# Optimization experiments

Hardware: AMD Instinct MI355X
Metric: run time of the kernel (lower is better)

## Reference

```python
import jax, jax.numpy as jnp
import numpy as np

T, B, M, H = 2048, 16, 512, 256
R_MIN, R_MAX, MAX_PHASE = 0.0, 1.0, 6.28


def setup_inputs() -> dict:
    key = jax.random.key(0)
    ks = jax.random.split(key, 10)
    inputs = jax.random.normal(ks[0], (T, B, M), dtype=jnp.float32)
    h_re = jnp.zeros((B, H), dtype=jnp.float32)
    h_im = jnp.zeros((B, H), dtype=jnp.float32)
    # parameter inits matching the torch module (stable |lambda| < 1)
    u1 = jax.random.uniform(ks[1], (H,), dtype=jnp.float32)
    nu_log = jnp.log(-0.5 * jnp.log(u1 * (R_MAX**2 - R_MIN**2) + R_MIN**2))
    u2 = jax.random.uniform(ks[2], (H,), dtype=jnp.float32)
    theta_log = jnp.log(MAX_PHASE * u2)
    lam = jnp.exp(-jnp.exp(nu_log) + 1j * jnp.exp(theta_log))
    gamma_log = jnp.log(jnp.sqrt(1.0 - jnp.abs(lam) ** 2))
    B_re = jax.random.normal(ks[3], (H, M), dtype=jnp.float32) / np.sqrt(2 * M)
    B_im = jax.random.normal(ks[4], (H, M), dtype=jnp.float32) / np.sqrt(2 * M)
    C_re = jax.random.normal(ks[5], (M, H), dtype=jnp.float32) / np.sqrt(H)
    C_im = jax.random.normal(ks[6], (M, H), dtype=jnp.float32) / np.sqrt(H)
    D = jax.random.normal(ks[7], (M,), dtype=jnp.float32)
    return {"inputs": inputs, "h_re": h_re, "h_im": h_im,
            "nu_log": nu_log, "theta_log": theta_log, "gamma_log": gamma_log,
            "B_re": B_re, "B_im": B_im, "C_re": C_re, "C_im": C_im, "D": D}


def reference(inputs, h_re, h_im, nu_log, theta_log, gamma_log,
              B_re, B_im, C_re, C_im, D):
    # diag_lambda = exp(-exp(nu) + i exp(theta)), shape [H]
    lam = jnp.exp(jnp.complex64(-jnp.exp(nu_log) + 1j * jnp.exp(theta_log)))
    B_norm = (B_re + 1j * B_im) * jnp.exp(gamma_log)[:, None]  # [H, M] complex
    C = C_re + 1j * C_im                                        # [M, H] complex
    h0 = (h_re + 1j * h_im).astype(jnp.complex64)               # [B, H]
    Bu = inputs.astype(jnp.complex64) @ B_norm.T                # [T, B, H] precomputed input drive

    def step(h, xs):
        bu_t, x_t = xs
        h = h * lam + bu_t                                      # [B, H]
        y = jnp.real(h @ C.T) + D * x_t                         # [B, M]
        return h, y

    h_final, outputs = jax.lax.scan(step, h0, (Bu, inputs))
    return outputs, h_final
```

## Files before the change

### kernel.cpp

```cpp
#include <hip/hip_runtime.h>
#include <hip/hip_bf16.h>
#include <math.h>

#define T_DIM 2048
#define B_DIM 16
#define M_DIM 512
#define H_DIM 256
#define KC 512
#define K_DIM 512
#define CHUNK 64
#define NCHUNK 32
#define NTILE 16

typedef unsigned short ushort_t;
typedef __attribute__((ext_vector_type(8))) short short8;
typedef __attribute__((ext_vector_type(8))) unsigned short ushort8;
typedef __attribute__((ext_vector_type(4))) float f32x4;

#define WS_CARRY 0
#define WS_WB_BF 262144
#define WS_WC_BF 393216
#define WS_XB    524288
#define WS_BU    8912896

__device__ inline int tidx(int n, int k) {
    return (((n >> 7) * 16 + (k >> 5)) << 12) + (((k >> 3) & 3) << 10)
         + ((n & 127) << 3) + (k & 7);
}

__device__ inline ushort_t f2bf(float f) {
    __hip_bfloat16 h = __float2bfloat16(f);
    return *reinterpret_cast<ushort_t*>(&h);
}
__device__ inline float bf2f(ushort_t u) {
    union { unsigned int i; float f; } v;
    v.i = ((unsigned int)u) << 16;
    return v.f;
}

__global__ __launch_bounds__(256) void prep_all(
        const float* __restrict__ X, ushort_t* __restrict__ Xb,
        const float* __restrict__ B_re, const float* __restrict__ B_im,
        const float* __restrict__ gamma_log,
        const float* __restrict__ C_re, const float* __restrict__ C_im,
        ushort_t* __restrict__ wb, ushort_t* __restrict__ wc) {
    int bid = blockIdx.x;
    if (bid < 8192) {
        int f = bid * 256 + threadIdx.x;
        int n = f >> 6, ko = f & 63;
        const float* p = X + (size_t)n * 512 + ko * 8;
        float4 a = *(const float4*)p;
        float4 b = *(const float4*)(p + 4);
        ushort8 u;
        u[0] = f2bf(a.x); u[1] = f2bf(a.y); u[2] = f2bf(a.z); u[3] = f2bf(a.w);
        u[4] = f2bf(b.x); u[5] = f2bf(b.y); u[6] = f2bf(b.z); u[7] = f2bf(b.w);
        *(ushort8*)(&Xb[(((n >> 7) * 16 + (ko >> 2)) << 12) + ((ko & 3) << 10)
                        + ((n & 127) << 3)]) = u;
    } else {
        int idx = (bid - 8192) * 256 + threadIdx.x;
        int e    = idx & 7;
        int slot = (idx >> 3) & 511;
        int row  = slot & 127;
        int ks   = slot >> 7;
        int t    = (idx >> 12) & 15;
        int blk  = idx >> 16;
        int j = blk * 128 + row;
        int k = t * 32 + ks * 8 + e;
        float v;
        if (j < 256) v = expf(gamma_log[j])       * B_re[j * 512 + k];
        else         v = expf(gamma_log[j - 256]) * B_im[(j - 256) * 512 + k];
        wb[idx] = f2bf(v);
        float w;
        if (k < 256) w =  C_re[j * 256 + k];
        else         w = -C_im[j * 256 + (k - 256)];
        wc[idx] = f2bf(w);
    }
}

template <int MODE>
__global__ __launch_bounds__(512) void gemm_mfma(
    const ushort_t* __restrict__ A, const ushort_t* __restrict__ W,
    void* __restrict__ Cv, const float* __restrict__ Dv,
    const ushort_t* __restrict__ Xb) {
    __shared__ ushort_t Asl[2][4][4096];
    __shared__ ushort_t Bsl[2][4][4096];
    const int tid = threadIdx.x;
    const int id = blockIdx.x;
    const int rb = ((id >> 4) << 3) + (id & 7);
    const int nb = (id >> 3) & 1;
    const int bm = rb << 8, bn = nb << 8;
    const int lane = tid & 63, wid = tid >> 6;
    const int wr  = (wid >> 2) << 7;
    const int wcc = (wid & 3) << 6;
    const int l16 = lane & 15, ksl = lane >> 4;

    f32x4 acc[MODE == 0 ? 4 : 8][MODE == 0 ? 8 : 4] = {};

    auto stage = [&](int t, int buf) {
#pragma unroll
        for (int q = 0; q < 2; ++q) {
#pragma unroll
            for (int kk = 0; kk < 2; ++kk) {
                size_t ab = ((size_t)((2 * rb + q) * NTILE + (2 * t + kk))) * 4096;
                __builtin_amdgcn_global_load_lds(
                    (const __attribute__((address_space(1))) void*)(A + ab + tid * 8),
                    (__attribute__((address_space(3))) void*)(&Asl[buf][q * 2 + kk][tid * 8]),
                    16, 0, 0);
                size_t bb = ((size_t)((2 * nb + q) * NTILE + (2 * t + kk))) * 4096;
                __builtin_amdgcn_global_load_lds(
                    (const __attribute__((address_space(1))) void*)(W + bb + tid * 8),
                    (__attribute__((address_space(3))) void*)(&Bsl[buf][q * 2 + kk][tid * 8]),
                    16, 0, 0);
            }
        }
    };

    stage(0, 0);
    __syncthreads();

    int cur = 0;
#pragma unroll 2
    for (int t = 0; t < 8; ++t) {
        const int nxt = cur ^ 1;
        if (t + 1 < 8) stage(t + 1, nxt);
#pragma unroll
        for (int kk = 0; kk < 2; ++kk) {
            short8 afr[8], bfr[4];
#pragma unroll
            for (int m = 0; m < 8; ++m) {
                int row = wr + m * 16 + l16;
                afr[m] = *(const short8*)(&Asl[cur][(row >> 7) * 2 + kk]
                                              [ksl * 1024 + (row & 127) * 8]);
            }
#pragma unroll
            for (int n = 0; n < 4; ++n) {
                int col = wcc + n * 16 + l16;
                bfr[n] = *(const short8*)(&Bsl[cur][(col >> 7) * 2 + kk]
                                              [ksl * 1024 + (col & 127) * 8]);
            }
            if constexpr (MODE == 0) {
#pragma unroll
                for (int i = 0; i < 4; ++i)
#pragma unroll
                    for (int j = 0; j < 8; ++j)
                        acc[i][j] = __builtin_amdgcn_mfma_f32_16x16x32_bf16(
                            bfr[i], afr[j], acc[i][j], 0, 0, 0);
            } else {
#pragma unroll
                for (int i = 0; i < 8; ++i)
#pragma unroll
                    for (int j = 0; j < 4; ++j)
                        acc[i][j] = __builtin_amdgcn_mfma_f32_16x16x32_bf16(
                            afr[i], bfr[j], acc[i][j], 0, 0, 0);
            }
        }
        __syncthreads();
        cur = nxt;
    }

    const int fr = (lane >> 4) << 2;
    if constexpr (MODE == 0) {
        ushort_t* Bu = (ushort_t*)Cv;
#pragma unroll
        for (int i = 0; i < 4; ++i) {
            int k0 = bn + wcc + i * 16 + fr;
#pragma unroll
            for (int j = 0; j < 8; ++j) {
                int n = bm + wr + j * 16 + l16;
                uint2 p;
                p.x = (unsigned int)f2bf(acc[i][j][0])
                    | ((unsigned int)f2bf(acc[i][j][1]) << 16);
                p.y = (unsigned int)f2bf(acc[i][j][2])
                    | ((unsigned int)f2bf(acc[i][j][3]) << 16);
                size_t off = ((size_t)((n >> 7) * 16 + (k0 >> 5)) << 12)
                           + (((k0 >> 3) & 3) << 10) + ((n & 127) << 3) + (k0 & 7);
                *(uint2*)(&Bu[off]) = p;
            }
        }
    } else {
#pragma unroll
        for (int i = 0; i < 8; ++i) {
#pragma unroll
            for (int j = 0; j < 4; ++j) {
#pragma unroll
                for (int r = 0; r < 4; ++r) {
                    int row = bm + wr + i * 16 + fr + r;
                    int col = bn + wcc + j * 16 + l16;
                    size_t o = (size_t)row * 512 + col;
                    ((float*)Cv)[o] = acc[i][j][r] + Dv[col] * bf2f(Xb[tidx(row, col)]);
                }
            }
        }
    }
}

__global__ __launch_bounds__(256) void scan_local(const float* __restrict__ nu_log,
        const float* __restrict__ theta_log, float* __restrict__ ws) {
    const int c = blockIdx.x;
    const int s = blockIdx.y;
    const int b = threadIdx.x >> 4;
    const int h0 = s * 32 + (threadIdx.x & 15) * 2;
    float lr[2], li[2];
#pragma unroll
    for (int q = 0; q < 2; ++q) {
        float nu = expf(nu_log[h0 + q]);
        float th = expf(theta_log[h0 + q]);
        float r  = expf(-nu);
        lr[q] = r * cosf(th); li[q] = r * sinf(th);
    }
    const ushort_t* Bu = (const ushort_t*)(ws + WS_BU);
    float hr[2] = {0.f, 0.f}, hi[2] = {0.f, 0.f};
    for (int l0 = 0; l0 < CHUNK; l0 += 8) {
        unsigned int vre[8], vim[8];
#pragma unroll
        for (int u = 0; u < 8; ++u) {
            int n = (c * CHUNK + l0 + u) * B_DIM + b;
            vre[u] = *(const unsigned int*)(&Bu[tidx(n, h0)]);
            vim[u] = *(const unsigned int*)(&Bu[tidx(n, h0 + 256)]);
        }
#pragma unroll
        for (int u = 0; u < 8; ++u) {
#pragma unroll
            for (int q = 0; q < 2; ++q) {
                float br = bf2f((ushort_t)(q ? (vre[u] >> 16) : (vre[u] & 0xffff)));
                float bi = bf2f((ushort_t)(q ? (vim[u] >> 16) : (vim[u] & 0xffff)));
                float nr = fmaf(lr[q], hr[q], fmaf(-li[q], hi[q], br));
                float ni = fmaf(lr[q], hi[q], fmaf(li[q], hr[q], bi));
                hr[q] = nr; hi[q] = ni;
            }
        }
    }
    size_t cb = (size_t)(c * B_DIM + b) * KC;
    *(float2*)(&ws[WS_CARRY + cb + h0])       = make_float2(hr[0], hr[1]);
    *(float2*)(&ws[WS_CARRY + cb + 256 + h0]) = make_float2(hi[0], hi[1]);
}

__global__ __launch_bounds__(256) void scan_carry(const float* __restrict__ nu_log,
        const float* __restrict__ theta_log, float* __restrict__ ws,
        const float* __restrict__ h_re, const float* __restrict__ h_im,
        float* __restrict__ out, int out_size) {
    const int b = blockIdx.x;
    const int h = threadIdx.x;
    const float nu = expf(nu_log[h]);
    const float th = expf(theta_log[h]);
    const float rL  = expf(-64.f * nu);
    const float thL = 64.f * th;
    const float Lr = rL * cosf(thL), Li = rL * sinf(thL);
    float cr = h_re[b * H_DIM + h], ci = h_im[b * H_DIM + h];
    for (int c = 0; c < NCHUNK; ++c) {
        size_t cidx = ((size_t)(c * B_DIM + b)) * KC + h;
        float sr = ws[WS_CARRY + cidx], si = ws[WS_CARRY + cidx + 256];
        ws[WS_CARRY + cidx]       = cr;
        ws[WS_CARRY + cidx + 256] = ci;
        float nr = fmaf(Lr, cr, fmaf(-Li, ci, sr));
        float ni = fmaf(Lr, ci, fmaf(Li, cr, si));
        cr = nr; ci = ni;
    }
    const size_t base = (size_t)T_DIM * B_DIM * M_DIM;
    const size_t idx  = (size_t)b * H_DIM + h;
    size_t ore = base + idx;
    size_t oim = base + (size_t)B_DIM * H_DIM + idx;
    if (ore < (size_t)out_size) out[ore] = cr;
    if (oim < (size_t)out_size) out[oim] = ci;
}

__global__ __launch_bounds__(256) void scan_apply(const float* __restrict__ nu_log,
        const float* __restrict__ theta_log, float* __restrict__ ws) {
    const int c = blockIdx.x;
    const int s = blockIdx.y;
    const int b = threadIdx.x >> 4;
    const int h0 = s * 32 + (threadIdx.x & 15) * 2;
    float lr[2], li[2];
#pragma unroll
    for (int q = 0; q < 2; ++q) {
        float nu = expf(nu_log[h0 + q]);
        float th = expf(theta_log[h0 + q]);
        float r  = expf(-nu);
        lr[q] = r * cosf(th); li[q] = r * sinf(th);
    }
    ushort_t* Bu = (ushort_t*)(ws + WS_BU);
    size_t cb = (size_t)(c * B_DIM + b) * KC;
    float2 f2r = *(const float2*)(&ws[WS_CARRY + cb + h0]);
    float2 f2i = *(const float2*)(&ws[WS_CARRY + cb + 256 + h0]);
    float hr[2] = {f2r.x, f2r.y}, hi[2] = {f2i.x, f2i.y};
    for (int l0 = 0; l0 < CHUNK; l0 += 8) {
        unsigned int vre[8], vim[8];
        int ire[8], iim[8];
#pragma unroll
        for (int u = 0; u < 8; ++u) {
            int n = (c * CHUNK + l0 + u) * B_DIM + b;
            ire[u] = tidx(n, h0);
            iim[u] = tidx(n, h0 + 256);
            vre[u] = *(const unsigned int*)(&Bu[ire[u]]);
            vim[u] = *(const unsigned int*)(&Bu[iim[u]]);
        }
#pragma unroll
        for (int u = 0; u < 8; ++u) {
#pragma unroll
            for (int q = 0; q < 2; ++q) {
                float br = bf2f((ushort_t)(q ? (vre[u] >> 16) : (vre[u] & 0xffff)));
                float bi = bf2f((ushort_t)(q ? (vim[u] >> 16) : (vim[u] & 0xffff)));
                float nr = fmaf(lr[q], hr[q], fmaf(-li[q], hi[q], br));
                float ni = fmaf(lr[q], hi[q], fmaf(li[q], hr[q], bi));
                hr[q] = nr; hi[q] = ni;
            }
            *(unsigned int*)(&Bu[ire[u]]) =
                (unsigned int)f2bf(hr[0]) | ((unsigned int)f2bf(hr[1]) << 16);
            *(unsigned int*)(&Bu[iim[u]]) =
                (unsigned int)f2bf(hi[0]) | ((unsigned int)f2bf(hi[1]) << 16);
        }
    }
}

extern "C" void kernel_launch(void* const* d_in, const int* in_sizes, int n_in,
                              void* d_out, int out_size, void* d_ws, size_t ws_size,
                              hipStream_t stream) {
    const float* inputs    = (const float*)d_in[0];
    const float* h_re      = (const float*)d_in[1];
    const float* h_im      = (const float*)d_in[2];
    const float* nu_log    = (const float*)d_in[3];
    const float* theta_log = (const float*)d_in[4];
    const float* gamma_log = (const float*)d_in[5];
    const float* B_re      = (const float*)d_in[6];
    const float* B_im      = (const float*)d_in[7];
    const float* C_re      = (const float*)d_in[8];
    const float* C_im      = (const float*)d_in[9];
    const float* Dv        = (const float*)d_in[10];
    float* out = (float*)d_out;
    float* ws  = (float*)d_ws;
    ushort_t* wb = (ushort_t*)(ws + WS_WB_BF);
    ushort_t* wc = (ushort_t*)(ws + WS_WC_BF);
    ushort_t* xb = (ushort_t*)(ws + WS_XB);
    ushort_t* bu = (ushort_t*)(ws + WS_BU);

    prep_all<<<9216, 256, 0, stream>>>(inputs, xb, B_re, B_im, gamma_log,
                                       C_re, C_im, wb, wc);

    gemm_mfma<0><<<256, 512, 0, stream>>>(xb, wb, (void*)bu, nullptr, nullptr);

    scan_local<<<dim3(NCHUNK, 8), 256, 0, stream>>>(nu_log, theta_log, ws);
    scan_carry<<<B_DIM, 256, 0, stream>>>(nu_log, theta_log, ws, h_re, h_im,
                                          out, out_size);
    scan_apply<<<dim3(NCHUNK, 8), 256, 0, stream>>>(nu_log, theta_log, ws);

    gemm_mfma<1><<<256, 512, 0, stream>>>(bu, wc, (void*)out, Dv, xb);
}
```

Measured before the change: 102.1 us.

## Fuse fp32-to-bf16 input conversion into first GEMM's A-tile load

Removes the separate pass that converted the fp32 inputs into a tiled bf16 copy. The first GEMM now loads fp32 input rows into registers, converts them to bf16 and writes them to LDS itself, with the register loads overlapped with the MFMA work of the current tile. The second GEMM's D*x skip term now reads the original fp32 inputs instead of the bf16 copy. This saves a full write and re-read of the converted activations and one kernel's worth of traffic, at the cost of register-staged loads in place of direct global-to-LDS loads and extra VALU conversion inside the GEMM.

```diff
diff --git a/kernel.cpp b/kernel.cpp
--- a/kernel.cpp
+++ b/kernel.cpp
@@ -20,7 +20,6 @@
 #define WS_CARRY 0
 #define WS_WB_BF 262144
 #define WS_WC_BF 393216
-#define WS_XB    524288
 #define WS_BU    8912896
 
 __device__ inline int tidx(int n, int k) {
@@ -38,50 +37,34 @@
     return v.f;
 }
 
-__global__ __launch_bounds__(256) void prep_all(
-        const float* __restrict__ X, ushort_t* __restrict__ Xb,
-        const float* __restrict__ B_re, const float* __restrict__ B_im,
-        const float* __restrict__ gamma_log,
-        const float* __restrict__ C_re, const float* __restrict__ C_im,
-        ushort_t* __restrict__ wb, ushort_t* __restrict__ wc) {
-    int bid = blockIdx.x;
-    if (bid < 8192) {
-        int f = bid * 256 + threadIdx.x;
-        int n = f >> 6, ko = f & 63;
-        const float* p = X + (size_t)n * 512 + ko * 8;
-        float4 a = *(const float4*)p;
-        float4 b = *(const float4*)(p + 4);
-        ushort8 u;
-        u[0] = f2bf(a.x); u[1] = f2bf(a.y); u[2] = f2bf(a.z); u[3] = f2bf(a.w);
-        u[4] = f2bf(b.x); u[5] = f2bf(b.y); u[6] = f2bf(b.z); u[7] = f2bf(b.w);
-        *(ushort8*)(&Xb[(((n >> 7) * 16 + (ko >> 2)) << 12) + ((ko & 3) << 10)
-                        + ((n & 127) << 3)]) = u;
-    } else {
-        int idx = (bid - 8192) * 256 + threadIdx.x;
-        int e    = idx & 7;
-        int slot = (idx >> 3) & 511;
-        int row  = slot & 127;
-        int ks   = slot >> 7;
-        int t    = (idx >> 12) & 15;
-        int blk  = idx >> 16;
-        int j = blk * 128 + row;
-        int k = t * 32 + ks * 8 + e;
-        float v;
-        if (j < 256) v = expf(gamma_log[j])       * B_re[j * 512 + k];
-        else         v = expf(gamma_log[j - 256]) * B_im[(j - 256) * 512 + k];
-        wb[idx] = f2bf(v);
-        float w;
-        if (k < 256) w =  C_re[j * 256 + k];
-        else         w = -C_im[j * 256 + (k - 256)];
-        wc[idx] = f2bf(w);
-    }
+__global__ void prep_w(const float* __restrict__ B_re, const float* __restrict__ B_im,
+                       const float* __restrict__ gamma_log,
+                       const float* __restrict__ C_re, const float* __restrict__ C_im,
+                       ushort_t* __restrict__ wb, ushort_t* __restrict__ wc) {
+    int idx = blockIdx.x * blockDim.x + threadIdx.x;
+    int e    = idx & 7;
+    int slot = (idx >> 3) & 511;
+    int row  = slot & 127;
+    int ks   = slot >> 7;
+    int t    = (idx >> 12) & 15;
+    int blk  = idx >> 16;
+    int j = blk * 128 + row;
+    int k = t * 32 + ks * 8 + e;
+    float v;
+    if (j < 256) v = expf(gamma_log[j])       * B_re[j * 512 + k];
+    else         v = expf(gamma_log[j - 256]) * B_im[(j - 256) * 512 + k];
+    wb[idx] = f2bf(v);
+    float w;
+    if (k < 256) w =  C_re[j * 256 + k];
+    else         w = -C_im[j * 256 + (k - 256)];
+    wc[idx] = f2bf(w);
 }
 
 template <int MODE>
 __global__ __launch_bounds__(512) void gemm_mfma(
-    const ushort_t* __restrict__ A, const ushort_t* __restrict__ W,
+    const void* __restrict__ Aptr, const ushort_t* __restrict__ W,
     void* __restrict__ Cv, const float* __restrict__ Dv,
-    const ushort_t* __restrict__ Xb) {
+    const float* __restrict__ X) {
     __shared__ ushort_t Asl[2][4][4096];
     __shared__ ushort_t Bsl[2][4][4096];
     const int tid = threadIdx.x;
@@ -94,35 +77,76 @@
     const int wcc = (wid & 3) << 6;
     const int l16 = lane & 15, ksl = lane >> 4;
 
+    const ushort_t* At = (const ushort_t*)Aptr;
+    const float*    Xf = (const float*)Aptr;
+
+    const int ar  = tid >> 1;
+    const int akh = (tid & 1) << 5;
+    const int asub = ((ar >> 7) << 1) + (tid & 1);
+    const int arow127 = ar & 127;
+
     f32x4 acc[MODE == 0 ? 4 : 8][MODE == 0 ? 8 : 4] = {};
-
-    auto stage = [&](int t, int buf) {
-#pragma unroll
-        for (int q = 0; q < 2; ++q) {
+    float4 av[8];
+
+    auto stageB = [&](int t, int buf) {
+#pragma unroll
+        for (int q = 0; q < 2; ++q)
 #pragma unroll
             for (int kk = 0; kk < 2; ++kk) {
-                size_t ab = ((size_t)((2 * rb + q) * NTILE + (2 * t + kk))) * 4096;
-                __builtin_amdgcn_global_load_lds(
-                    (const __attribute__((address_space(1))) void*)(A + ab + tid * 8),
-                    (__attribute__((address_space(3))) void*)(&Asl[buf][q * 2 + kk][tid * 8]),
-                    16, 0, 0);
                 size_t bb = ((size_t)((2 * nb + q) * NTILE + (2 * t + kk))) * 4096;
                 __builtin_amdgcn_global_load_lds(
                     (const __attribute__((address_space(1))) void*)(W + bb + tid * 8),
                     (__attribute__((address_space(3))) void*)(&Bsl[buf][q * 2 + kk][tid * 8]),
                     16, 0, 0);
             }
-        }
     };
-
-    stage(0, 0);
+    auto stageA = [&](int t, int buf) {
+#pragma unroll
+        for (int q = 0; q < 2; ++q)
+#pragma unroll
+            for (int kk = 0; kk < 2; ++kk) {
+                size_t ab = ((size_t)((2 * rb + q) * NTILE + (2 * t + kk))) * 4096;
+                __builtin_amdgcn_global_load_lds(
+                    (const __attribute__((address_space(1))) void*)(At + ab + tid * 8),
+                    (__attribute__((address_space(3))) void*)(&Asl[buf][q * 2 + kk][tid * 8]),
+                    16, 0, 0);
+            }
+    };
+    auto loadA = [&](int t) {
+        const float* p = Xf + (size_t)(bm + ar) * 512 + t * 64 + akh;
+#pragma unroll
+        for (int i = 0; i < 8; ++i) av[i] = *(const float4*)(p + i * 4);
+    };
+    auto writeA = [&](int buf) {
+#pragma unroll
+        for (int i = 0; i < 4; ++i) {
+            float4 a = av[2 * i], b = av[2 * i + 1];
+            ushort8 u;
+            u[0] = f2bf(a.x); u[1] = f2bf(a.y); u[2] = f2bf(a.z); u[3] = f2bf(a.w);
+            u[4] = f2bf(b.x); u[5] = f2bf(b.y); u[6] = f2bf(b.z); u[7] = f2bf(b.w);
+            *(ushort8*)(&Asl[buf][asub][(i * 128 + arow127) * 8]) = u;
+        }
+    };
+
+    if constexpr (MODE == 0) {
+        stageB(0, 0);
+        loadA(0);
+        writeA(0);
+    } else {
+        stageA(0, 0);
+        stageB(0, 0);
+    }
     __syncthreads();
 
     int cur = 0;
 #pragma unroll 2
     for (int t = 0; t < 8; ++t) {
         const int nxt = cur ^ 1;
-        if (t + 1 < 8) stage(t + 1, nxt);
+        if (t + 1 < 8) {
+            stageB(t + 1, nxt);
+            if constexpr (MODE == 0) loadA(t + 1);
+            else                     stageA(t + 1, nxt);
+        }
 #pragma unroll
         for (int kk = 0; kk < 2; ++kk) {
             short8 afr[8], bfr[4];
@@ -154,6 +178,7 @@
                             afr[i], bfr[j], acc[i][j], 0, 0, 0);
             }
         }
+        if constexpr (MODE == 0) { if (t + 1 < 8) writeA(nxt); }
         __syncthreads();
         cur = nxt;
     }
@@ -187,7 +212,7 @@
                     int row = bm + wr + i * 16 + fr + r;
                     int col = bn + wcc + j * 16 + l16;
                     size_t o = (size_t)row * 512 + col;
-                    ((float*)Cv)[o] = acc[i][j][r] + Dv[col] * bf2f(Xb[tidx(row, col)]);
+                    ((float*)Cv)[o] = acc[i][j][r] + Dv[col] * X[o];
                 }
             }
         }
@@ -330,18 +355,16 @@
     float* ws  = (float*)d_ws;
     ushort_t* wb = (ushort_t*)(ws + WS_WB_BF);
     ushort_t* wc = (ushort_t*)(ws + WS_WC_BF);
-    ushort_t* xb = (ushort_t*)(ws + WS_XB);
     ushort_t* bu = (ushort_t*)(ws + WS_BU);
 
-    prep_all<<<9216, 256, 0, stream>>>(inputs, xb, B_re, B_im, gamma_log,
-                                       C_re, C_im, wb, wc);
-
-    gemm_mfma<0><<<256, 512, 0, stream>>>(xb, wb, (void*)bu, nullptr, nullptr);
+    prep_w<<<1024, 256, 0, stream>>>(B_re, B_im, gamma_log, C_re, C_im, wb, wc);
+
+    gemm_mfma<0><<<256, 512, 0, stream>>>(inputs, wb, (void*)bu, nullptr, inputs);
 
     scan_local<<<dim3(NCHUNK, 8), 256, 0, stream>>>(nu_log, theta_log, ws);
     scan_carry<<<B_DIM, 256, 0, stream>>>(nu_log, theta_log, ws, h_re, h_im,
                                           out, out_size);
     scan_apply<<<dim3(NCHUNK, 8), 256, 0, stream>>>(nu_log, theta_log, ws);
 
-    gemm_mfma<1><<<256, 512, 0, stream>>>(bu, wc, (void*)out, Dv, xb);
-}
+    gemm_mfma<1><<<256, 512, 0, stream>>>(bu, wc, (void*)out, Dv, inputs);
+}
```

New measurement: 103.7 us. Within noise of the previous version (+1.6%).

## Fuse chunk-carry propagation into scan_apply, removing the serial carry kernel

Applied to the files above, without the earlier changes.

Removes the separate scan_carry kernel that walked the 32 chunk summaries serially per batch. Each scan_apply block now recomputes its own incoming carry by folding all preceding chunk summaries with lambda^64, and the last chunk writes the final hidden state. This saves a kernel launch and a serial dependency stage. In exchange it adds redundant carry work, up to 31 steps for later chunks, and makes the load uneven across blocks.

```diff
diff --git a/kernel.cpp b/kernel.cpp
--- a/kernel.cpp
+++ b/kernel.cpp
@@ -235,54 +235,44 @@
     *(float2*)(&ws[WS_CARRY + cb + 256 + h0]) = make_float2(hi[0], hi[1]);
 }
 
-__global__ __launch_bounds__(256) void scan_carry(const float* __restrict__ nu_log,
+__global__ __launch_bounds__(256) void scan_apply(const float* __restrict__ nu_log,
         const float* __restrict__ theta_log, float* __restrict__ ws,
         const float* __restrict__ h_re, const float* __restrict__ h_im,
         float* __restrict__ out, int out_size) {
-    const int b = blockIdx.x;
-    const int h = threadIdx.x;
-    const float nu = expf(nu_log[h]);
-    const float th = expf(theta_log[h]);
-    const float rL  = expf(-64.f * nu);
-    const float thL = 64.f * th;
-    const float Lr = rL * cosf(thL), Li = rL * sinf(thL);
-    float cr = h_re[b * H_DIM + h], ci = h_im[b * H_DIM + h];
-    for (int c = 0; c < NCHUNK; ++c) {
-        size_t cidx = ((size_t)(c * B_DIM + b)) * KC + h;
-        float sr = ws[WS_CARRY + cidx], si = ws[WS_CARRY + cidx + 256];
-        ws[WS_CARRY + cidx]       = cr;
-        ws[WS_CARRY + cidx + 256] = ci;
-        float nr = fmaf(Lr, cr, fmaf(-Li, ci, sr));
-        float ni = fmaf(Lr, ci, fmaf(Li, cr, si));
-        cr = nr; ci = ni;
-    }
-    const size_t base = (size_t)T_DIM * B_DIM * M_DIM;
-    const size_t idx  = (size_t)b * H_DIM + h;
-    size_t ore = base + idx;
-    size_t oim = base + (size_t)B_DIM * H_DIM + idx;
-    if (ore < (size_t)out_size) out[ore] = cr;
-    if (oim < (size_t)out_size) out[oim] = ci;
-}
-
-__global__ __launch_bounds__(256) void scan_apply(const float* __restrict__ nu_log,
-        const float* __restrict__ theta_log, float* __restrict__ ws) {
     const int c = blockIdx.x;
     const int s = blockIdx.y;
     const int b = threadIdx.x >> 4;
     const int h0 = s * 32 + (threadIdx.x & 15) * 2;
-    float lr[2], li[2];
+    float lr[2], li[2], Lr[2], Li[2];
 #pragma unroll
     for (int q = 0; q < 2; ++q) {
         float nu = expf(nu_log[h0 + q]);
         float th = expf(theta_log[h0 + q]);
         float r  = expf(-nu);
         lr[q] = r * cosf(th); li[q] = r * sinf(th);
+        float rL  = expf(-64.f * nu);
+        float thL = 64.f * th;
+        Lr[q] = rL * cosf(thL); Li[q] = rL * sinf(thL);
+    }
+    float hr[2], hi[2];
+#pragma unroll
+    for (int q = 0; q < 2; ++q) {
+        hr[q] = h_re[b * H_DIM + h0 + q];
+        hi[q] = h_im[b * H_DIM + h0 + q];
+    }
+    for (int j = 0; j < c; ++j) {
+        size_t cb = (size_t)(j * B_DIM + b) * KC;
+        float2 sre = *(const float2*)(&ws[WS_CARRY + cb + h0]);
+        float2 sim = *(const float2*)(&ws[WS_CARRY + cb + 256 + h0]);
+        float sr[2] = {sre.x, sre.y}, si[2] = {sim.x, sim.y};
+#pragma unroll
+        for (int q = 0; q < 2; ++q) {
+            float nr = fmaf(Lr[q], hr[q], fmaf(-Li[q], hi[q], sr[q]));
+            float ni = fmaf(Lr[q], hi[q], fmaf(Li[q], hr[q], si[q]));
+            hr[q] = nr; hi[q] = ni;
+        }
     }
     ushort_t* Bu = (ushort_t*)(ws + WS_BU);
-    size_t cb = (size_t)(c * B_DIM + b) * KC;
-    float2 f2r = *(const float2*)(&ws[WS_CARRY + cb + h0]);
-    float2 f2i = *(const float2*)(&ws[WS_CARRY + cb + 256 + h0]);
-    float hr[2] = {f2r.x, f2r.y}, hi[2] = {f2i.x, f2i.y};
     for (int l0 = 0; l0 < CHUNK; l0 += 8) {
         unsigned int vre[8], vim[8];
         int ire[8], iim[8];
@@ -308,6 +298,17 @@
                 (unsigned int)f2bf(hr[0]) | ((unsigned int)f2bf(hr[1]) << 16);
             *(unsigned int*)(&Bu[iim[u]]) =
                 (unsigned int)f2bf(hi[0]) | ((unsigned int)f2bf(hi[1]) << 16);
+        }
+    }
+    if (c == NCHUNK - 1) {
+        const size_t base = (size_t)T_DIM * B_DIM * M_DIM;
+#pragma unroll
+        for (int q = 0; q < 2; ++q) {
+            size_t idx = (size_t)b * H_DIM + h0 + q;
+            size_t ore = base + idx;
+            size_t oim = base + (size_t)B_DIM * H_DIM + idx;
+            if (ore < (size_t)out_size) out[ore] = hr[q];
+            if (oim < (size_t)out_size) out[oim] = hi[q];
         }
     }
 }
@@ -339,9 +340,8 @@
     gemm_mfma<0><<<256, 512, 0, stream>>>(xb, wb, (void*)bu, nullptr, nullptr);
 
     scan_local<<<dim3(NCHUNK, 8), 256, 0, stream>>>(nu_log, theta_log, ws);
-    scan_carry<<<B_DIM, 256, 0, stream>>>(nu_log, theta_log, ws, h_re, h_im,
-                                          out, out_size);
-    scan_apply<<<dim3(NCHUNK, 8), 256, 0, stream>>>(nu_log, theta_log, ws);
+    scan_apply<<<dim3(NCHUNK, 8), 256, 0, stream>>>(nu_log, theta_log, ws,
+                                                    h_re, h_im, out, out_size);
 
     gemm_mfma<1><<<256, 512, 0, stream>>>(bu, wc, (void*)out, Dv, xb);
 }
```

After: 107.6 us. +5.4%, slower.
